# Performance work log

Measured on AMD Instinct MI355X. Metric: run time of the kernel, lower is better.

The kernel has to match this reference:

```python
import jax, jax.numpy as jnp
import numpy as np

N_NODES = 100000
N_EDGES = 1280000
D_IN = 64
D_HID = 64


def _sage_conv(x, src, dst, deg, Wl, bl, Wr):
    # gather source-node features per edge, scatter-mean to destination nodes
    msg = x[src]                                            # [E, d]
    agg = jax.ops.segment_sum(msg, dst, num_segments=N_NODES)  # [N, d]
    mean = agg / deg                                        # [N, d]
    # PyG SAGEConv: lin_l(aggregated) + lin_r(root); bias lives in lin_l
    return mean @ Wl.T + bl + x @ Wr.T


def setup_inputs() -> dict:
    key = jax.random.key(0)
    ks = jax.random.split(key, 10)
    x = jax.random.normal(ks[0], (N_NODES, D_IN), dtype=jnp.float32)
    edge_index = jax.random.randint(ks[1], (2, N_EDGES), 0, N_NODES, dtype=jnp.int64)
    s = 1.0 / np.sqrt(D_IN)
    W1l = jax.random.uniform(ks[2], (D_HID, D_IN), jnp.float32, -s, s)
    W1r = jax.random.uniform(ks[3], (D_HID, D_IN), jnp.float32, -s, s)
    b1 = jax.random.uniform(ks[4], (D_HID,), jnp.float32, -s, s)
    s2 = 1.0 / np.sqrt(D_HID)
    W2l = jax.random.uniform(ks[5], (D_HID, D_HID), jnp.float32, -s2, s2)
    W2r = jax.random.uniform(ks[6], (D_HID, D_HID), jnp.float32, -s2, s2)
    b2 = jax.random.uniform(ks[7], (D_HID,), jnp.float32, -s2, s2)
    Wh = jax.random.uniform(ks[8], (1, D_HID), jnp.float32, -s2, s2)
    bh = jax.random.uniform(ks[9], (1,), jnp.float32, -s2, s2)
    return {"x": x, "edge_index": edge_index, "W1l": W1l, "W1r": W1r, "b1": b1,
            "W2l": W2l, "W2r": W2r, "b2": b2, "Wh": Wh, "bh": bh}


def reference(x, edge_index, W1l, W1r, b1, W2l, W2r, b2, Wh, bh):
    src, dst = edge_index[0], edge_index[1]
    # in-degree for mean aggregation (clamped to avoid div-by-zero)
    deg = jax.ops.segment_sum(jnp.ones((N_EDGES,), jnp.float32), dst,
                              num_segments=N_NODES)
    deg = jnp.maximum(deg, 1.0)[:, None]                    # [N, 1]
    h = jax.nn.relu(_sage_conv(x, src, dst, deg, W1l, b1, W1r))
    h = jax.nn.relu(_sage_conv(h, src, dst, deg, W2l, b2, W2r))
    out = (h @ Wh.T + bh)[:, 0]                             # [N]
    return out, h
```

## Files before the change

kernel.cpp:

```cpp
#include <hip/hip_runtime.h>

#define N_NODES 100000
#define N_EDGES 1280000
#define D 64
#define NPAD 102400
#define CAP 48
#define NBUCK 391
#define AB 313
#define CVB 1024
#define NTILES 1563
#define XQ (N_NODES * 16)

typedef __attribute__((ext_vector_type(8))) short bf16x8;
typedef __attribute__((ext_vector_type(4))) float f32x4;
typedef __attribute__((ext_vector_type(2))) float f32x2;

__device__ __forceinline__ unsigned short f2bf(float f) {
    union { float f; unsigned u; } c; c.f = f;
    unsigned u = c.u;
    return (unsigned short)((u + 0x7FFF + ((u >> 16) & 1)) >> 16);
}
__device__ __forceinline__ float bf2f(unsigned short s) {
    union { unsigned u; float f; } c; c.u = ((unsigned)s) << 16;
    return c.f;
}
__device__ __forceinline__ float fp8d(unsigned b) {
    unsigned t = ((b & 0x80u) << 24) | ((b & 0x7fu) << 20);
    union { unsigned u; float f; } c; c.u = t;
    return c.f * 1.32922799578491587e36f;
}
__device__ __forceinline__ unsigned char f2fp8(float f) {
    f = fminf(fmaxf(f, -448.f), 448.f);
    float g = f * 7.52316384526264005e-37f;
    union { float f; unsigned u; } c; c.f = g;
    unsigned gb = c.u;
    unsigned r = (((gb & 0x7fffffffu) + 0x7ffffu + ((gb >> 20) & 1u)) >> 20) & 0x7fu;
    return (unsigned char)(((gb >> 24) & 0x80u) | r);
}

__global__ __launch_bounds__(512) void prep_kernel(
    const float* __restrict__ x,
    const int* __restrict__ src, const int* __restrict__ dst,
    const float* __restrict__ W1l, const float* __restrict__ W1r,
    const float* __restrict__ W2l, const float* __restrict__ W2r,
    unsigned short* __restrict__ xb, unsigned short* __restrict__ h1b,
    unsigned char* __restrict__ x8, unsigned char* __restrict__ h8,
    unsigned short* __restrict__ wb,
    int* __restrict__ sorted, int* __restrict__ exclT)
{
    __shared__ int cntA[392];
    __shared__ int excl[512];
    __shared__ int stage_pk[4096];

    const int t   = threadIdx.x;
    const int bid = blockIdx.x;

    if (bid < AB) {
        const int e0 = bid * 4096;
        const int cbatch = min(4096, N_EDGES - e0);

        if (t < 392) cntA[t] = 0;
        __syncthreads();

        int mb[8], mr[8], mpk[8];
#pragma unroll
        for (int i = 0; i < 8; ++i) {
            int idx = i * 512 + t;
            mb[i] = -1;
            if (idx < cbatch) {
                int e = e0 + idx;
                int s = src[e], d = dst[e];
                int b = d >> 8;
                mb[i]  = b;
                mpk[i] = (s << 8) | (d & 255);
                mr[i]  = atomicAdd(&cntA[b], 1);
            }
        }
        __syncthreads();

        excl[t] = (t < 392) ? cntA[t] : 0;
        __syncthreads();
        for (int off = 1; off < 512; off <<= 1) {
            int u = (t >= off) ? excl[t - off] : 0;
            __syncthreads();
            excl[t] += u;
            __syncthreads();
        }

#pragma unroll
        for (int i = 0; i < 8; ++i) {
            if (mb[i] >= 0) {
                int b = mb[i];
                stage_pk[excl[b] - cntA[b] + mr[i]] = mpk[i];
            }
        }
        __syncthreads();

#pragma unroll
        for (int i = 0; i < 8; ++i) {
            int idx = i * 512 + t;
            if (idx < cbatch) sorted[e0 + idx] = stage_pk[idx];
        }
        if (t < 392) exclT[bid * 392 + t] = excl[t] - cntA[t];
    } else {
        const int gtid = (bid - AB) * 512 + t;
        const int gsz  = CVB * 512;
        const int TOT  = XQ + 32 + 4096;
        for (int i = gtid; i < TOT; i += gsz) {
            if (i < XQ) {
                float4 v = ((const float4*)x)[i];
                ((ushort4*)xb)[i] = make_ushort4(f2bf(v.x), f2bf(v.y), f2bf(v.z), f2bf(v.w));
                ((uchar4*)x8)[i]  = make_uchar4(f2fp8(v.x), f2fp8(v.y), f2fp8(v.z), f2fp8(v.w));
            } else if (i < XQ + 32) {
                int k = i - XQ;
                if (k < 16) {
                    ((ushort4*)xb)[(size_t)N_NODES * 16 + k] = make_ushort4(0,0,0,0);
                    ((unsigned*)x8)[(size_t)N_NODES * 16 + k] = 0u;
                } else {
                    ((ushort4*)h1b)[(size_t)N_NODES * 16 + (k - 16)] = make_ushort4(0,0,0,0);
                    ((unsigned*)h8)[(size_t)N_NODES * 16 + (k - 16)] = 0u;
                }
            } else {
                int wf = i - XQ - 32;
                int m = wf >> 10, k = wf & 1023;
                const float* s = (m == 0) ? W1l : (m == 1) ? W1r : (m == 2) ? W2l : W2r;
                float4 v = ((const float4*)s)[k];
                ((ushort4*)wb)[m * 1024 + k] =
                    make_ushort4(f2bf(v.x), f2bf(v.y), f2bf(v.z), f2bf(v.w));
            }
        }
    }
}

__global__ __launch_bounds__(512) void binB_kernel(const int* __restrict__ sorted,
                                                   const int* __restrict__ exclT,
                                                   int* __restrict__ csr,
                                                   int* __restrict__ deg) {
    __shared__ int cur[256];
    __shared__ int lcsr[256 * CAP];
    __shared__ int scan[512];
    __shared__ int segstart[314];
    __shared__ int segsrc[313];

    const int t = threadIdx.x;
    const int k = blockIdx.x;

    if (t < 256) cur[t] = 0;

    int cnt = 0, s0 = 0;
    if (t < AB) {
        s0  = exclT[t * 392 + k];
        cnt = exclT[t * 392 + k + 1] - s0;
    }
    scan[t] = (t < AB) ? cnt : 0;
    __syncthreads();
    for (int off = 1; off < 512; off <<= 1) {
        int u = (t >= off) ? scan[t - off] : 0;
        __syncthreads();
        scan[t] += u;
        __syncthreads();
    }
    if (t < AB) {
        segstart[t] = scan[t] - cnt;
        segsrc[t]   = t * 4096 + s0;
    }
    if (t == AB - 1) segstart[AB] = scan[AB - 1];
    __syncthreads();

    const int Tk = segstart[AB];
    for (int i = t; i < Tk; i += 512) {
        int lo = 0, hi = AB;
        while (hi - lo > 1) {
            int mid = (lo + hi) >> 1;
            if (segstart[mid] <= i) lo = mid; else hi = mid;
        }
        int pk = sorted[segsrc[lo] + (i - segstart[lo])];
        int nl = pk & 255;
        int s  = pk >> 8;
        int r  = atomicAdd(&cur[nl], 1);
        if (r < CAP) lcsr[nl * CAP + r] = s;
    }
    __syncthreads();

    const int base = k * 256;
    for (int i = t; i < 256 * CAP; i += 512)
        csr[(size_t)base * CAP + i] = lcsr[i];
    if (t < 256) deg[base + t] = cur[t];
}

template <int LAYER>
__global__ __launch_bounds__(512) void layer_kernel(
    const int* __restrict__ csr, const int* __restrict__ deg_g,
    const unsigned char*  __restrict__ feat8,
    const unsigned short* __restrict__ root_b,
    const unsigned short* __restrict__ wl_b,
    const float* __restrict__ bl,
    const unsigned short* __restrict__ wr_b,
    unsigned short* __restrict__ hout_b,
    unsigned char*  __restrict__ hout8,
    float* __restrict__ hout_f,
    const float* __restrict__ Wh, const float* __restrict__ bh,
    float* __restrict__ out)
{
    __shared__ __align__(16) char lds[18432 + 2048];
    unsigned short* sA = (unsigned short*)lds;
    unsigned short* sX = sA + 64 * 72;
    float* sH    = (float*)lds;
    float* spart = (float*)(lds + 18432);

    const int tid = threadIdx.x;
    const int n0  = blockIdx.x * 64;

#pragma unroll
    for (int i = 0; i < 2; ++i) {
        int idx = tid + 512 * i;
        int row = idx >> 4, c4 = idx & 15;
        int n = n0 + row;
        ushort4 x4 = make_ushort4(0, 0, 0, 0);
        if (n < N_NODES) x4 = ((const ushort4*)root_b)[(size_t)n * 16 + c4];
        *(ushort4*)(sX + row * 72 + c4 * 4) = x4;
    }

    const unsigned* fb = (const unsigned*)feat8;
    const int l   = tid & 15;
    const int grp = tid >> 4;
#pragma unroll 1
    for (int p = 0; p < 2; ++p) {
        int rloc = p * 32 + grp;
        int n = n0 + rloc;
        int deg = (n < N_NODES) ? deg_g[n] : 0;
        int len = (deg < CAP) ? deg : CAP;
        const int* row = csr + (size_t)n * CAP;
        f32x2 a01 = {0.f, 0.f}, a23 = {0.f, 0.f};
        for (int cb = 0; cb < len; cb += 16) {
            int idxl = cb + l;
            int id = (idxl < len) ? row[idxl] : N_NODES;
            unsigned v[16];
#pragma unroll
            for (int i = 0; i < 16; ++i)
                v[i] = fb[(size_t)__shfl(id, i, 16) * 16 + l];
#pragma unroll
            for (int i = 0; i < 16; ++i) {
#if __has_builtin(__builtin_amdgcn_cvt_pk_f32_fp8)
                a01 += __builtin_amdgcn_cvt_pk_f32_fp8((int)v[i], false);
                a23 += __builtin_amdgcn_cvt_pk_f32_fp8((int)v[i], true);
#else
                f32x2 p0 = {fp8d(v[i] & 255), fp8d((v[i] >> 8) & 255)};
                f32x2 p1 = {fp8d((v[i] >> 16) & 255), fp8d(v[i] >> 24)};
                a01 += p0;
                a23 += p1;
#endif
            }
        }
        float inv = 1.0f / fmaxf((float)deg, 1.0f);
        *(ushort4*)(sA + rloc * 72 + l * 4) =
            make_ushort4(f2bf(a01.x * inv), f2bf(a01.y * inv),
                         f2bf(a23.x * inv), f2bf(a23.y * inv));
    }
    __syncthreads();

    const int w8 = tid >> 6;
    const int rt = w8 & 3, ch = w8 >> 2;
    const int l64 = tid & 63;
    const int rowl = l64 & 15, quad = l64 >> 4;

    const unsigned short* ab = sA + (rt * 16 + rowl) * 72 + quad * 8;
    const unsigned short* xb = sX + (rt * 16 + rowl) * 72 + quad * 8;
    bf16x8 am0 = *(const bf16x8*)(ab);
    bf16x8 am1 = *(const bf16x8*)(ab + 32);
    bf16x8 ax0 = *(const bf16x8*)(xb);
    bf16x8 ax1 = *(const bf16x8*)(xb + 32);
    __syncthreads();

    f32x4 acc2[2];
    float bj2[2];
#pragma unroll
    for (int j2 = 0; j2 < 2; ++j2) {
        int jt = ch * 2 + j2;
        const unsigned short* wlp = wl_b + (jt * 16 + rowl) * 64 + quad * 8;
        const unsigned short* wrp = wr_b + (jt * 16 + rowl) * 64 + quad * 8;
        bf16x8 b0 = *(const bf16x8*)(wlp);
        bf16x8 b1 = *(const bf16x8*)(wlp + 32);
        bf16x8 b2 = *(const bf16x8*)(wrp);
        bf16x8 b3 = *(const bf16x8*)(wrp + 32);
        f32x4 acc = {0.f, 0.f, 0.f, 0.f};
        acc = __builtin_amdgcn_mfma_f32_16x16x32_bf16(am0, b0, acc, 0, 0, 0);
        acc = __builtin_amdgcn_mfma_f32_16x16x32_bf16(am1, b1, acc, 0, 0, 0);
        acc = __builtin_amdgcn_mfma_f32_16x16x32_bf16(ax0, b2, acc, 0, 0, 0);
        acc = __builtin_amdgcn_mfma_f32_16x16x32_bf16(ax1, b3, acc, 0, 0, 0);
        acc2[j2] = acc;
        bj2[j2] = bl[jt * 16 + rowl];
    }

#pragma unroll
    for (int j2 = 0; j2 < 2; ++j2) {
        int jt = ch * 2 + j2;
#pragma unroll
        for (int r = 0; r < 4; ++r) {
            int node = rt * 16 + quad * 4 + r;
            sH[node * 68 + jt * 16 + rowl] = fmaxf(acc2[j2][r] + bj2[j2], 0.f);
        }
    }
    __syncthreads();

    if (LAYER == 2) {
        int node = tid >> 3, q = tid & 7;
        float p = 0.f;
#pragma unroll
        for (int c = 0; c < 2; ++c) {
            float4 hv = *(const float4*)(sH + node * 68 + q * 8 + c * 4);
            float4 wv = ((const float4*)Wh)[q * 2 + c];
            p += hv.x * wv.x + hv.y * wv.y + hv.z * wv.z + hv.w * wv.w;
        }
        spart[tid] = p;
    }

#pragma unroll
    for (int i = 0; i < 2; ++i) {
        int idx = tid + 512 * i;
        int row = idx >> 4, c4 = idx & 15;
        int n = n0 + row;
        if (n < N_NODES) {
            const float* hp = sH + row * 68 + c4 * 4;
            if (LAYER == 1) {
                ((ushort4*)hout_b)[(size_t)n * 16 + c4] =
                    make_ushort4(f2bf(hp[0]), f2bf(hp[1]), f2bf(hp[2]), f2bf(hp[3]));
                ((uchar4*)hout8)[(size_t)n * 16 + c4] =
                    make_uchar4(f2fp8(hp[0]), f2fp8(hp[1]), f2fp8(hp[2]), f2fp8(hp[3]));
            } else {
                ((float4*)hout_f)[(size_t)n * 16 + c4] =
                    make_float4(hp[0], hp[1], hp[2], hp[3]);
            }
        }
    }

    if (LAYER == 2) {
        __syncthreads();
        if (tid < 64) {
            int n = n0 + tid;
            if (n < N_NODES) {
                float s = bh[0];
#pragma unroll
                for (int k = 0; k < 8; ++k) s += spart[tid * 8 + k];
                out[n] = s;
            }
        }
    }
}

extern "C" void kernel_launch(void* const* d_in, const int* in_sizes, int n_in,
                              void* d_out, int out_size, void* d_ws, size_t ws_size,
                              hipStream_t stream) {
    const float* x   = (const float*)d_in[0];
    const int*   ei  = (const int*)d_in[1];
    const int*   src = ei;
    const int*   dst = ei + N_EDGES;
    const float* W1l = (const float*)d_in[2];
    const float* W1r = (const float*)d_in[3];
    const float* b1  = (const float*)d_in[4];
    const float* W2l = (const float*)d_in[5];
    const float* W2r = (const float*)d_in[6];
    const float* b2  = (const float*)d_in[7];
    const float* Wh  = (const float*)d_in[8];
    const float* bh  = (const float*)d_in[9];

    float* out   = (float*)d_out;
    float* h_out = out + N_NODES;

    int* wsi = (int*)d_ws;
    int* deg = wsi;
    int* csr = deg + NPAD;
    unsigned short* wb  = (unsigned short*)(csr + NBUCK * 256 * CAP);
    unsigned short* x_b = wb + 16384;
    unsigned short* h1b = x_b + (size_t)(N_NODES + 1) * D;
    unsigned char*  x8  = (unsigned char*)(h1b + (size_t)(N_NODES + 1) * D);
    unsigned char*  h8  = x8 + (size_t)(N_NODES + 1) * D;
    int* sorted = (int*)h1b;
    int* exclT  = sorted + AB * 4096;

    unsigned short* w1l_b = wb;
    unsigned short* w1r_b = wb + 4096;
    unsigned short* w2l_b = wb + 8192;
    unsigned short* w2r_b = wb + 12288;

    prep_kernel<<<AB + CVB, 512, 0, stream>>>(
        x, src, dst, W1l, W1r, W2l, W2r, x_b, h1b, x8, h8, wb, sorted, exclT);

    binB_kernel<<<NBUCK, 512, 0, stream>>>(sorted, exclT, csr, deg);

    layer_kernel<1><<<NTILES, 512, 0, stream>>>(
        csr, deg, x8, x_b, w1l_b, b1, w1r_b, h1b, h8, nullptr,
        nullptr, nullptr, nullptr);
    layer_kernel<2><<<NTILES, 512, 0, stream>>>(
        csr, deg, h8, h1b, w2l_b, b2, w2r_b, nullptr, nullptr, h_out,
        Wh, bh, out);
}
```

Measured before the change: 184.3 us.

## Halve layer tile to 32 nodes, gather 8-byte fp8 chunks, trim CSR copy-out

Result: no change. 181.7 us (-1.4%).

```diff
diff --git a/kernel.cpp b/kernel.cpp
--- a/kernel.cpp
+++ b/kernel.cpp
@@ -8,7 +8,7 @@
 #define NBUCK 391
 #define AB 313
 #define CVB 1024
-#define NTILES 1563
+#define NT32 3125
 #define XQ (N_NODES * 16)
 
 typedef __attribute__((ext_vector_type(8))) short bf16x8;
@@ -137,7 +137,7 @@
                                                    int* __restrict__ csr,
                                                    int* __restrict__ deg) {
     __shared__ int cur[256];
-    __shared__ int lcsr[256 * CAP];
+    __shared__ __align__(16) int lcsr[256 * CAP];
     __shared__ int scan[512];
     __shared__ int segstart[314];
     __shared__ int segsrc[313];
@@ -183,8 +183,15 @@
     __syncthreads();
 
     const int base = k * 256;
-    for (int i = t; i < 256 * CAP; i += 512)
-        csr[(size_t)base * CAP + i] = lcsr[i];
+    for (int i = t; i < 4096; i += 512) {
+        int r = i >> 4, c = i & 15;
+        if (c < 12) {
+            int lenr = min(cur[r], CAP);
+            if (c * 4 < lenr)
+                *(int4*)(csr + (size_t)(base + r) * CAP + c * 4) =
+                    *(const int4*)(lcsr + r * CAP + c * 4);
+        }
+    }
     if (t < 256) deg[base + t] = cur[t];
 }
 
@@ -202,108 +209,105 @@
     const float* __restrict__ Wh, const float* __restrict__ bh,
     float* __restrict__ out)
 {
-    __shared__ __align__(16) char lds[18432 + 2048];
+    __shared__ __align__(16) char lds[10240];
     unsigned short* sA = (unsigned short*)lds;
-    unsigned short* sX = sA + 64 * 72;
+    unsigned short* sX = sA + 32 * 72;
     float* sH    = (float*)lds;
-    float* spart = (float*)(lds + 18432);
+    float* spart = (float*)(lds + 9216);
 
     const int tid = threadIdx.x;
-    const int n0  = blockIdx.x * 64;
-
-#pragma unroll
-    for (int i = 0; i < 2; ++i) {
-        int idx = tid + 512 * i;
-        int row = idx >> 4, c4 = idx & 15;
-        int n = n0 + row;
-        ushort4 x4 = make_ushort4(0, 0, 0, 0);
-        if (n < N_NODES) x4 = ((const ushort4*)root_b)[(size_t)n * 16 + c4];
+    const int n0  = blockIdx.x * 32;
+
+    {
+        int row = tid >> 4, c4 = tid & 15;
+        ushort4 x4 = ((const ushort4*)root_b)[(n0 + row) * 16 + c4];
         *(ushort4*)(sX + row * 72 + c4 * 4) = x4;
     }
 
-    const unsigned* fb = (const unsigned*)feat8;
-    const int l   = tid & 15;
-    const int grp = tid >> 4;
-#pragma unroll 1
-    for (int p = 0; p < 2; ++p) {
-        int rloc = p * 32 + grp;
-        int n = n0 + rloc;
-        int deg = (n < N_NODES) ? deg_g[n] : 0;
-        int len = (deg < CAP) ? deg : CAP;
-        const int* row = csr + (size_t)n * CAP;
-        f32x2 a01 = {0.f, 0.f}, a23 = {0.f, 0.f};
+    {
+        const uint2* fb2 = (const uint2*)feat8;
+        const int g   = tid >> 4;
+        const int l   = tid & 15;
+        const int h   = l >> 3;
+        const int lo  = l & 7;
+        const int n   = n0 + g;
+        const int dg  = deg_g[n];
+        const int len = (dg < CAP) ? dg : CAP;
+        const int* rp = csr + n * CAP;
+        f32x2 a0 = {0.f, 0.f}, a1 = {0.f, 0.f}, a2 = {0.f, 0.f}, a3 = {0.f, 0.f};
         for (int cb = 0; cb < len; cb += 16) {
             int idxl = cb + l;
-            int id = (idxl < len) ? row[idxl] : N_NODES;
-            unsigned v[16];
-#pragma unroll
-            for (int i = 0; i < 16; ++i)
-                v[i] = fb[(size_t)__shfl(id, i, 16) * 16 + l];
-#pragma unroll
-            for (int i = 0; i < 16; ++i) {
+            int id = (idxl < len) ? rp[idxl] : N_NODES;
+            uint2 w[8];
+#pragma unroll
+            for (int i = 0; i < 8; ++i)
+                w[i] = fb2[(__shfl(id, 2 * i + h, 16) << 3) + lo];
+#pragma unroll
+            for (int i = 0; i < 8; ++i) {
 #if __has_builtin(__builtin_amdgcn_cvt_pk_f32_fp8)
-                a01 += __builtin_amdgcn_cvt_pk_f32_fp8((int)v[i], false);
-                a23 += __builtin_amdgcn_cvt_pk_f32_fp8((int)v[i], true);
+                a0 += __builtin_amdgcn_cvt_pk_f32_fp8((int)w[i].x, false);
+                a1 += __builtin_amdgcn_cvt_pk_f32_fp8((int)w[i].x, true);
+                a2 += __builtin_amdgcn_cvt_pk_f32_fp8((int)w[i].y, false);
+                a3 += __builtin_amdgcn_cvt_pk_f32_fp8((int)w[i].y, true);
 #else
-                f32x2 p0 = {fp8d(v[i] & 255), fp8d((v[i] >> 8) & 255)};
-                f32x2 p1 = {fp8d((v[i] >> 16) & 255), fp8d(v[i] >> 24)};
-                a01 += p0;
-                a23 += p1;
+                f32x2 p0 = {fp8d(w[i].x & 255), fp8d((w[i].x >> 8) & 255)};
+                f32x2 p1 = {fp8d((w[i].x >> 16) & 255), fp8d(w[i].x >> 24)};
+                f32x2 p2 = {fp8d(w[i].y & 255), fp8d((w[i].y >> 8) & 255)};
+                f32x2 p3 = {fp8d((w[i].y >> 16) & 255), fp8d(w[i].y >> 24)};
+                a0 += p0; a1 += p1; a2 += p2; a3 += p3;
 #endif
             }
         }
-        float inv = 1.0f / fmaxf((float)deg, 1.0f);
-        *(ushort4*)(sA + rloc * 72 + l * 4) =
-            make_ushort4(f2bf(a01.x * inv), f2bf(a01.y * inv),
-                         f2bf(a23.x * inv), f2bf(a23.y * inv));
+        a0.x += __shfl_xor(a0.x, 8); a0.y += __shfl_xor(a0.y, 8);
+        a1.x += __shfl_xor(a1.x, 8); a1.y += __shfl_xor(a1.y, 8);
+        a2.x += __shfl_xor(a2.x, 8); a2.y += __shfl_xor(a2.y, 8);
+        a3.x += __shfl_xor(a3.x, 8); a3.y += __shfl_xor(a3.y, 8);
+        float inv = 1.0f / fmaxf((float)dg, 1.0f);
+        if (h == 0) {
+            *(ushort4*)(sA + g * 72 + lo * 8) =
+                make_ushort4(f2bf(a0.x * inv), f2bf(a0.y * inv),
+                             f2bf(a1.x * inv), f2bf(a1.y * inv));
+            *(ushort4*)(sA + g * 72 + lo * 8 + 4) =
+                make_ushort4(f2bf(a2.x * inv), f2bf(a2.y * inv),
+                             f2bf(a3.x * inv), f2bf(a3.y * inv));
+        }
     }
     __syncthreads();
 
     const int w8 = tid >> 6;
-    const int rt = w8 & 3, ch = w8 >> 2;
+    const int rt = w8 & 1, jt = w8 >> 1;
     const int l64 = tid & 63;
     const int rowl = l64 & 15, quad = l64 >> 4;
 
-    const unsigned short* ab = sA + (rt * 16 + rowl) * 72 + quad * 8;
-    const unsigned short* xb = sX + (rt * 16 + rowl) * 72 + quad * 8;
-    bf16x8 am0 = *(const bf16x8*)(ab);
-    bf16x8 am1 = *(const bf16x8*)(ab + 32);
-    bf16x8 ax0 = *(const bf16x8*)(xb);
-    bf16x8 ax1 = *(const bf16x8*)(xb + 32);
-    __syncthreads();
-
-    f32x4 acc2[2];
-    float bj2[2];
-#pragma unroll
-    for (int j2 = 0; j2 < 2; ++j2) {
-        int jt = ch * 2 + j2;
-        const unsigned short* wlp = wl_b + (jt * 16 + rowl) * 64 + quad * 8;
-        const unsigned short* wrp = wr_b + (jt * 16 + rowl) * 64 + quad * 8;
-        bf16x8 b0 = *(const bf16x8*)(wlp);
-        bf16x8 b1 = *(const bf16x8*)(wlp + 32);
-        bf16x8 b2 = *(const bf16x8*)(wrp);
-        bf16x8 b3 = *(const bf16x8*)(wrp + 32);
-        f32x4 acc = {0.f, 0.f, 0.f, 0.f};
-        acc = __builtin_amdgcn_mfma_f32_16x16x32_bf16(am0, b0, acc, 0, 0, 0);
-        acc = __builtin_amdgcn_mfma_f32_16x16x32_bf16(am1, b1, acc, 0, 0, 0);
-        acc = __builtin_amdgcn_mfma_f32_16x16x32_bf16(ax0, b2, acc, 0, 0, 0);
-        acc = __builtin_amdgcn_mfma_f32_16x16x32_bf16(ax1, b3, acc, 0, 0, 0);
-        acc2[j2] = acc;
-        bj2[j2] = bl[jt * 16 + rowl];
-    }
-
-#pragma unroll
-    for (int j2 = 0; j2 < 2; ++j2) {
-        int jt = ch * 2 + j2;
-#pragma unroll
-        for (int r = 0; r < 4; ++r) {
-            int node = rt * 16 + quad * 4 + r;
-            sH[node * 68 + jt * 16 + rowl] = fmaxf(acc2[j2][r] + bj2[j2], 0.f);
-        }
-    }
-    __syncthreads();
-
-    if (LAYER == 2) {
+    const unsigned short* ap = sA + (rt * 16 + rowl) * 72 + quad * 8;
+    const unsigned short* xp = sX + (rt * 16 + rowl) * 72 + quad * 8;
+    bf16x8 am0 = *(const bf16x8*)(ap);
+    bf16x8 am1 = *(const bf16x8*)(ap + 32);
+    bf16x8 ax0 = *(const bf16x8*)(xp);
+    bf16x8 ax1 = *(const bf16x8*)(xp + 32);
+    __syncthreads();
+
+    const unsigned short* wlp = wl_b + (jt * 16 + rowl) * 64 + quad * 8;
+    const unsigned short* wrp = wr_b + (jt * 16 + rowl) * 64 + quad * 8;
+    bf16x8 b0 = *(const bf16x8*)(wlp);
+    bf16x8 b1 = *(const bf16x8*)(wlp + 32);
+    bf16x8 b2 = *(const bf16x8*)(wrp);
+    bf16x8 b3 = *(const bf16x8*)(wrp + 32);
+    f32x4 acc = {0.f, 0.f, 0.f, 0.f};
+    acc = __builtin_amdgcn_mfma_f32_16x16x32_bf16(am0, b0, acc, 0, 0, 0);
+    acc = __builtin_amdgcn_mfma_f32_16x16x32_bf16(am1, b1, acc, 0, 0, 0);
+    acc = __builtin_amdgcn_mfma_f32_16x16x32_bf16(ax0, b2, acc, 0, 0, 0);
+    acc = __builtin_amdgcn_mfma_f32_16x16x32_bf16(ax1, b3, acc, 0, 0, 0);
+    float bj = bl[jt * 16 + rowl];
+
+#pragma unroll
+    for (int r = 0; r < 4; ++r) {
+        int node = rt * 16 + quad * 4 + r;
+        sH[node * 68 + jt * 16 + rowl] = fmaxf(acc[r] + bj, 0.f);
+    }
+    __syncthreads();
+
+    if (LAYER == 2 && tid < 256) {
         int node = tid >> 3, q = tid & 7;
         float p = 0.f;
 #pragma unroll
@@ -315,35 +319,28 @@
         spart[tid] = p;
     }
 
-#pragma unroll
-    for (int i = 0; i < 2; ++i) {
-        int idx = tid + 512 * i;
-        int row = idx >> 4, c4 = idx & 15;
+    {
+        int row = tid >> 4, c4 = tid & 15;
         int n = n0 + row;
-        if (n < N_NODES) {
-            const float* hp = sH + row * 68 + c4 * 4;
-            if (LAYER == 1) {
-                ((ushort4*)hout_b)[(size_t)n * 16 + c4] =
-                    make_ushort4(f2bf(hp[0]), f2bf(hp[1]), f2bf(hp[2]), f2bf(hp[3]));
-                ((uchar4*)hout8)[(size_t)n * 16 + c4] =
-                    make_uchar4(f2fp8(hp[0]), f2fp8(hp[1]), f2fp8(hp[2]), f2fp8(hp[3]));
-            } else {
-                ((float4*)hout_f)[(size_t)n * 16 + c4] =
-                    make_float4(hp[0], hp[1], hp[2], hp[3]);
-            }
+        const float* hp = sH + row * 68 + c4 * 4;
+        if (LAYER == 1) {
+            ((ushort4*)hout_b)[n * 16 + c4] =
+                make_ushort4(f2bf(hp[0]), f2bf(hp[1]), f2bf(hp[2]), f2bf(hp[3]));
+            ((uchar4*)hout8)[n * 16 + c4] =
+                make_uchar4(f2fp8(hp[0]), f2fp8(hp[1]), f2fp8(hp[2]), f2fp8(hp[3]));
+        } else {
+            ((float4*)hout_f)[n * 16 + c4] =
+                make_float4(hp[0], hp[1], hp[2], hp[3]);
         }
     }
 
     if (LAYER == 2) {
         __syncthreads();
-        if (tid < 64) {
-            int n = n0 + tid;
-            if (n < N_NODES) {
-                float s = bh[0];
-#pragma unroll
-                for (int k = 0; k < 8; ++k) s += spart[tid * 8 + k];
-                out[n] = s;
-            }
+        if (tid < 32) {
+            float s = bh[0];
+#pragma unroll
+            for (int q = 0; q < 8; ++q) s += spart[tid * 8 + q];
+            out[n0 + tid] = s;
         }
     }
 }
@@ -388,10 +385,10 @@
 
     binB_kernel<<<NBUCK, 512, 0, stream>>>(sorted, exclT, csr, deg);
 
-    layer_kernel<1><<<NTILES, 512, 0, stream>>>(
+    layer_kernel<1><<<NT32, 512, 0, stream>>>(
         csr, deg, x8, x_b, w1l_b, b1, w1r_b, h1b, h8, nullptr,
         nullptr, nullptr, nullptr);
-    layer_kernel<2><<<NTILES, 512, 0, stream>>>(
+    layer_kernel<2><<<NT32, 512, 0, stream>>>(
         csr, deg, h8, h1b, w2l_b, b2, w2r_b, nullptr, nullptr, h_out,
         Wh, bh, out);
 }
```
